# Kernel optimization log

Measured on AMD Instinct MI355X. Metric: run time of the kernel, lower is better.

## Reference

```python
import jax, jax.numpy as jnp
import numpy as np

N, L, D, H, MLP_MULT = 2, 384, 512, 8, 4
HD = D // H
DM = D * MLP_MULT
EPS = 1e-5


def _linear_params(key, out_dim, in_dim, scale=0.02):
    kw, kb = jax.random.split(key)
    w = jax.random.normal(kw, (out_dim, in_dim), jnp.float32) * scale
    b = jax.random.normal(kb, (out_dim,), jnp.float32) * scale
    return w, b


def setup_inputs() -> dict:
    key = jax.random.key(0)
    ks = jax.random.split(key, 12)
    x = jax.random.normal(ks[0], (N, L, D), jnp.float32)
    mem = jax.random.normal(ks[1], (N, L, D), jnp.float32)
    pairwise_distances = jax.random.normal(ks[2], (N, L, L, D), jnp.float32)
    mem_padding_mask = jax.random.randint(ks[3], (N, L), 0, 2).astype(bool)
    qw, qb = _linear_params(ks[4], D, D)
    kvw, kvb = _linear_params(ks[5], 2 * D, D)
    pw, pb = _linear_params(ks[6], D, D)
    edw, edb = _linear_params(ks[7], H, D)
    w1, b1 = _linear_params(ks[8], DM, D)
    w2, b2 = _linear_params(ks[9], DM, DM)
    w3, b3 = _linear_params(ks[10], D, DM)
    return {
        'x': x, 'mem': mem, 'pairwise_distances': pairwise_distances,
        'mem_padding_mask': mem_padding_mask,
        'qw': qw, 'qb': qb, 'kvw': kvw, 'kvb': kvb, 'pw': pw, 'pb': pb,
        'edw': edw, 'edb': edb,
        'ln1_g': jnp.ones((D,), jnp.float32), 'ln1_b': jnp.zeros((D,), jnp.float32),
        'ln2_g': jnp.ones((D,), jnp.float32), 'ln2_b': jnp.zeros((D,), jnp.float32),
        'w1': w1, 'b1': b1, 'w2': w2, 'b2': b2, 'w3': w3, 'b3': b3,
    }


def _layernorm(x, g, b):
    m = jnp.mean(x, axis=-1, keepdims=True)
    v = jnp.mean((x - m) ** 2, axis=-1, keepdims=True)
    return (x - m) * jax.lax.rsqrt(v + EPS) * g + b


def reference(x, mem, pairwise_distances, mem_padding_mask,
              qw, qb, kvw, kvb, pw, pb, edw, edb,
              ln1_g, ln1_b, ln2_g, ln2_b,
              w1, b1, w2, b2, w3, b3):
    scale = HD ** -0.5
    a_in = _layernorm(x, ln1_g, ln1_b)
    a_mem = _layernorm(mem, ln1_g, ln1_b)

    q = (a_in @ qw.T + qb).reshape(N, L, H, HD).transpose(0, 2, 1, 3)   # (N,H,L1,HD)
    kv = (a_mem @ kvw.T + kvb).reshape(N, L, 2, H, HD)
    k = kv[:, :, 0].transpose(0, 2, 1, 3)                               # (N,H,L2,HD)
    v = kv[:, :, 1].transpose(0, 2, 1, 3)

    scores = jnp.einsum('bhid,bhjd->bhij', q, k) * scale                # (N,H,L1,L2)

    # T5-style relative position bias from pairwise distances
    bias = (pairwise_distances @ edw.T + edb)                            # (N,L1,L2,H)
    scores = scores + bias.transpose(0, 3, 1, 2)

    # padding mask (True = padded); rows that are fully padded get a zero
    # mask instead (then their output is zeroed after attention)
    all_pad = jnp.all(mem_padding_mask, axis=-1)                         # (N,)
    neg_inf = jnp.asarray(-jnp.inf, scores.dtype)
    mask = jnp.where(mem_padding_mask[:, None, None, :], neg_inf, 0.0)
    mask = jnp.where(all_pad[:, None, None, None], 0.0, mask)
    scores = scores + mask

    attn = jax.nn.softmax(scores, axis=-1)
    out = jnp.einsum('bhij,bhjd->bhid', attn, v)                         # (N,H,L1,HD)
    out = out * (~all_pad)[:, None, None, None]
    out = out.transpose(0, 2, 1, 3).reshape(N, L, D)

    x = x + (out @ pw.T + pb)

    h = _layernorm(x, ln2_g, ln2_b)
    h = jax.nn.silu(h @ w1.T + b1)
    h = jax.nn.silu(h @ w2.T + b2)
    h = h @ w3.T + b3
    return x + h
```

## Files before the change

### kernel.cpp

```cpp
#include <hip/hip_runtime.h>
#include <hip/hip_bf16.h>
#include <math.h>

#define NB   2
#define LSEQ 384
#define DMODEL 512
#define NH   8
#define HD2  64
#define DMLP 2048
#define LL2  (LSEQ*LSEQ)
#define ROWS (NB*LSEQ)

using bf16x8 = __attribute__((ext_vector_type(8))) short;
using f32x4  = __attribute__((ext_vector_type(4))) float;

__device__ __forceinline__ unsigned short f2bf(float f) {
    union { __hip_bfloat16 h; unsigned short u; } cv;
    cv.h = __float2bfloat16(f);
    return cv.u;
}

__device__ __forceinline__ void gload_lds16(const void* g, void* l) {
    __builtin_amdgcn_global_load_lds(
        (const __attribute__((address_space(1))) void*)g,
        (__attribute__((address_space(3))) void*)l, 16, 0, 0);
}

__device__ __forceinline__ void wait_vmcnt(int rem) {
    if (rem >= 3)      asm volatile("s_waitcnt vmcnt(12)" ::: "memory");
    else if (rem == 2) asm volatile("s_waitcnt vmcnt(8)"  ::: "memory");
    else if (rem == 1) asm volatile("s_waitcnt vmcnt(4)"  ::: "memory");
    else               asm volatile("s_waitcnt vmcnt(0)"  ::: "memory");
}

__global__ __launch_bounds__(256) void cvt_all_kernel(
        const float* __restrict__ s0, const float* __restrict__ s1,
        const float* __restrict__ s2, const float* __restrict__ s3,
        const float* __restrict__ s4, const float* __restrict__ s5,
        const float* __restrict__ edw,
        unsigned short* __restrict__ d0, unsigned short* __restrict__ d1,
        unsigned short* __restrict__ d2, unsigned short* __restrict__ d3,
        unsigned short* __restrict__ d4, unsigned short* __restrict__ d5,
        unsigned short* __restrict__ edwb) {
    const int stride = gridDim.x * blockDim.x;
    const int t0 = blockIdx.x * blockDim.x + threadIdx.x;
    const float* srcs[6] = {s0, s1, s2, s3, s4, s5};
    unsigned short* dsts[6] = {d0, d1, d2, d3, d4, d5};
    const int nf4[6] = {DMODEL*DMODEL/4, 2*DMODEL*DMODEL/4, DMODEL*DMODEL/4,
                        DMLP*DMODEL/4, DMLP*DMLP/4, DMLP*DMODEL/4};
    #pragma unroll
    for (int a = 0; a < 6; a++) {
        const float* s = srcs[a];
        unsigned short* d = dsts[a];
        for (int i = t0; i < nf4[a]; i += stride) {
            float4 v = *(const float4*)(s + (size_t)i * 4);
            ushort4 o = {f2bf(v.x), f2bf(v.y), f2bf(v.z), f2bf(v.w)};
            *(ushort4*)(d + (size_t)i * 4) = o;
        }
    }
    for (int i = t0; i < 16 * 512 / 4; i += stride) {
        int row = (i * 4) >> 9;
        float4 v = {0.f, 0.f, 0.f, 0.f};
        if (row < 8) v = *(const float4*)(edw + (size_t)i * 4);
        ushort4 o = {f2bf(v.x), f2bf(v.y), f2bf(v.z), f2bf(v.w)};
        *(ushort4*)(edwb + (size_t)i * 4) = o;
    }
}

__global__ __launch_bounds__(256) void ln_kernel(const float* __restrict__ src0,
                                                 const float* __restrict__ src1,
                                                 const float* __restrict__ g,
                                                 const float* __restrict__ b,
                                                 unsigned short* __restrict__ dst0,
                                                 unsigned short* __restrict__ dst1) {
    int lane = threadIdx.x & 63;
    int row  = blockIdx.x * 4 + (threadIdx.x >> 6);
    const float* src = (row < ROWS) ? src0 : src1;
    unsigned short* dst = (row < ROWS) ? dst0 : dst1;
    int r2 = (row < ROWS) ? row : row - ROWS;
    const float* p = src + (size_t)r2 * DMODEL + lane * 8;
    float4 v0 = *(const float4*)p;
    float4 v1 = *(const float4*)(p + 4);
    float s  = v0.x + v0.y + v0.z + v0.w + v1.x + v1.y + v1.z + v1.w;
    float ss = v0.x*v0.x + v0.y*v0.y + v0.z*v0.z + v0.w*v0.w
             + v1.x*v1.x + v1.y*v1.y + v1.z*v1.z + v1.w*v1.w;
    #pragma unroll
    for (int o = 32; o; o >>= 1) { s += __shfl_xor(s, o); ss += __shfl_xor(ss, o); }
    float m   = s * (1.0f / DMODEL);
    float var = ss * (1.0f / DMODEL) - m * m;
    float r   = rsqrtf(var + 1e-5f);
    float4 g0 = *(const float4*)(g + lane * 8);
    float4 g1 = *(const float4*)(g + lane * 8 + 4);
    float4 b0 = *(const float4*)(b + lane * 8);
    float4 b1 = *(const float4*)(b + lane * 8 + 4);
    unsigned short* q = dst + (size_t)r2 * DMODEL + lane * 8;
    ushort4 lo = {f2bf((v0.x - m) * r * g0.x + b0.x), f2bf((v0.y - m) * r * g0.y + b0.y),
                  f2bf((v0.z - m) * r * g0.z + b0.z), f2bf((v0.w - m) * r * g0.w + b0.w)};
    ushort4 hi = {f2bf((v1.x - m) * r * g1.x + b1.x), f2bf((v1.y - m) * r * g1.y + b1.y),
                  f2bf((v1.z - m) * r * g1.z + b1.z), f2bf((v1.w - m) * r * g1.w + b1.w)};
    *(ushort4*)q = lo;
    *(ushort4*)(q + 4) = hi;
}

__global__ __launch_bounds__(256) void bias_mfma(const float* __restrict__ pd,
                                                 const unsigned short* __restrict__ edwb,
                                                 const float* __restrict__ edb,
                                                 const int* __restrict__ mask,
                                                 float* __restrict__ biasb) {
    __shared__ float Asb[2][64 * 64];
    const int tid = threadIdx.x;
    const int lane = tid & 63, w = tid >> 6;
    const int T = blockIdx.x;
    const size_t row0 = (size_t)T * 64;
    const int n = T / 2304;
    const int rem64 = (T - n * 2304) * 64;
    const int i = rem64 / LSEQ, j0 = rem64 % LSEQ;

    int pad = 1;
    for (int j = lane; j < LSEQ; j += 64) pad &= (mask[n * LSEQ + j] != 0) ? 1 : 0;
    unsigned long long bal = __ballot(pad);
    const int ap = (bal == ~0ull) ? 1 : 0;

    int rr[4], sc[4];
    #pragma unroll
    for (int q = 0; q < 4; q++) {
        int s = q * 256 + tid;
        rr[q] = s >> 4;
        int cs = s & 15;
        sc[q] = (cs & 8) | ((cs & 7) ^ (rr[q] & 7));
    }

    const int c = lane & 15, g = lane >> 4;
    f32x4 acc = {};

    #pragma unroll
    for (int q = 0; q < 4; q++)
        gload_lds16(pd + (row0 + rr[q]) * DMODEL + sc[q] * 4, &Asb[0][(q * 256 + tid) * 4]);
    __syncthreads();

    for (int kc = 0; kc < 8; kc++) {
        if (kc < 7) {
            const int nb = (kc + 1) & 1;
            #pragma unroll
            for (int q = 0; q < 4; q++)
                gload_lds16(pd + (row0 + rr[q]) * DMODEL + (kc + 1) * 64 + sc[q] * 4,
                            &Asb[nb][(q * 256 + tid) * 4]);
        }
        const float* Ab = &Asb[kc & 1][0];
        #pragma unroll
        for (int ks = 0; ks < 2; ks++) {
            const int ch0 = (8 * ks) | ((2 * g) ^ (c & 7));
            const int ch1 = (8 * ks) | ((2 * g + 1) ^ (c & 7));
            float4 a0 = *(const float4*)&Ab[(w * 16 + c) * 64 + ch0 * 4];
            float4 a1 = *(const float4*)&Ab[(w * 16 + c) * 64 + ch1 * 4];
            bf16x8 af;
            af[0] = (short)f2bf(a0.x); af[1] = (short)f2bf(a0.y);
            af[2] = (short)f2bf(a0.z); af[3] = (short)f2bf(a0.w);
            af[4] = (short)f2bf(a1.x); af[5] = (short)f2bf(a1.y);
            af[6] = (short)f2bf(a1.z); af[7] = (short)f2bf(a1.w);
            bf16x8 bfv = *(const bf16x8*)&edwb[c * 512 + kc * 64 + ks * 32 + g * 8];
            acc = __builtin_amdgcn_mfma_f32_16x16x32_bf16(af, bfv, acc, 0, 0, 0);
        }
        if (kc < 7) __syncthreads();
    }

    if (c < 8) {
        const float eb = edb[c];
        const int jj = j0 + w * 16 + g * 4;
        int4 mv = *(const int4*)&mask[n * LSEQ + jj];
        const float NEGINF = -__builtin_inff();
        float4 o;
        o.x = acc[0] + eb + ((!ap && mv.x) ? NEGINF : 0.0f);
        o.y = acc[1] + eb + ((!ap && mv.y) ? NEGINF : 0.0f);
        o.z = acc[2] + eb + ((!ap && mv.z) ? NEGINF : 0.0f);
        o.w = acc[3] + eb + ((!ap && mv.w) ? NEGINF : 0.0f);
        *(float4*)&biasb[(size_t)(n * 8 + c) * LL2 + (size_t)i * LSEQ + jj] = o;
    }
}

template<int ACT, int RES, int OBF>
__device__ __forceinline__ void gemm_body(const unsigned short* __restrict__ A,
        const unsigned short* __restrict__ W, const float* __restrict__ bv,
        const float* __restrict__ Rsd, void* __restrict__ Cv,
        int Nn, int K, int m0, int n0, short* As, short* Ws) {
    const int tid  = threadIdx.x;
    const int lane = tid & 63, w = tid >> 6;
    const int wr = w >> 1, wc = w & 1;
    const int s0 = tid, s1 = 256 + tid;
    const int r0 = s0 >> 3, c0 = ((s0 & 7) ^ (r0 & 7)) << 3;
    const int r1 = s1 >> 3, c1 = ((s1 & 7) ^ (r1 & 7)) << 3;
    const unsigned short* ag0 = A + (size_t)(m0 + r0) * K + c0;
    const unsigned short* ag1 = A + (size_t)(m0 + r1) * K + c1;
    const unsigned short* wg0 = W + (size_t)(n0 + r0) * K + c0;
    const unsigned short* wg1 = W + (size_t)(n0 + r1) * K + c1;

    f32x4 acc[2][2] = {};
    const int lc = lane & 15, lr = lane >> 4;
    const int KT = K >> 6;

    #pragma unroll
    for (int t = 0; t < 4; t++) {
        const int b = t * 4096, k0 = t << 6;
        gload_lds16(ag0 + k0, &As[b + s0 * 8]);
        gload_lds16(ag1 + k0, &As[b + s1 * 8]);
        gload_lds16(wg0 + k0, &Ws[b + s0 * 8]);
        gload_lds16(wg1 + k0, &Ws[b + s1 * 8]);
    }

    for (int t = 0; t < KT; t++) {
        int rem = KT - 1 - t; if (rem > 3) rem = 3;
        wait_vmcnt(rem);
        __builtin_amdgcn_s_barrier();
        __builtin_amdgcn_sched_barrier(0);
        const int cur = (t & 3) * 4096;
        bf16x8 af[2][2], bfr[2][2];
        #pragma unroll
        for (int m = 0; m < 2; m++) {
            const int rra = wr * 32 + m * 16 + lc;
            #pragma unroll
            for (int kk = 0; kk < 2; kk++) {
                const int cc = (lr + kk * 4) ^ (rra & 7);
                af[m][kk] = *(const bf16x8*)&As[cur + rra * 64 + cc * 8];
            }
        }
        #pragma unroll
        for (int nn = 0; nn < 2; nn++) {
            const int rrb = wc * 32 + nn * 16 + lc;
            #pragma unroll
            for (int kk = 0; kk < 2; kk++) {
                const int cc = (lr + kk * 4) ^ (rrb & 7);
                bfr[nn][kk] = *(const bf16x8*)&Ws[cur + rrb * 64 + cc * 8];
            }
        }
        #pragma unroll
        for (int m = 0; m < 2; m++)
            #pragma unroll
            for (int nn = 0; nn < 2; nn++) {
                acc[m][nn] = __builtin_amdgcn_mfma_f32_16x16x32_bf16(af[m][0], bfr[nn][0], acc[m][nn], 0, 0, 0);
                acc[m][nn] = __builtin_amdgcn_mfma_f32_16x16x32_bf16(af[m][1], bfr[nn][1], acc[m][nn], 0, 0, 0);
            }
        if (t + 4 < KT) {
            __builtin_amdgcn_sched_barrier(0);
            __builtin_amdgcn_s_barrier();
            const int b = cur, k0 = (t + 4) << 6;
            gload_lds16(ag0 + k0, &As[b + s0 * 8]);
            gload_lds16(ag1 + k0, &As[b + s1 * 8]);
            gload_lds16(wg0 + k0, &Ws[b + s0 * 8]);
            gload_lds16(wg1 + k0, &Ws[b + s1 * 8]);
        }
    }

    #pragma unroll
    for (int nn = 0; nn < 2; nn++) {
        int gcol = n0 + wc * 32 + nn * 16 + lc;
        float bb = bv[gcol];
        #pragma unroll
        for (int m = 0; m < 2; m++) {
            #pragma unroll
            for (int r = 0; r < 4; r++) {
                int grow = m0 + wr * 32 + m * 16 + lr * 4 + r;
                float o = acc[m][nn][r] + bb;
                if (ACT) o = o / (1.0f + expf(-o));
                if (RES) o += Rsd[(size_t)grow * Nn + gcol];
                if (OBF) ((unsigned short*)Cv)[(size_t)grow * Nn + gcol] = f2bf(o);
                else     ((float*)Cv)[(size_t)grow * Nn + gcol] = o;
            }
        }
    }
}

template<int ACT, int RES, int OBF>
__global__ __launch_bounds__(256) void mfma_gemm(const unsigned short* __restrict__ A,
                                                 const unsigned short* __restrict__ W,
                                                 const float* __restrict__ bv,
                                                 const float* __restrict__ Rsd,
                                                 void* __restrict__ Cv, int Nn, int K) {
    __shared__ short As[4 * 4096];
    __shared__ short Ws[4 * 4096];
    gemm_body<ACT, RES, OBF>(A, W, bv, Rsd, Cv, Nn, K, blockIdx.y * 64, blockIdx.x * 64, As, Ws);
}

__global__ __launch_bounds__(256) void qkv_gemm(const unsigned short* __restrict__ a_in,
                                                const unsigned short* __restrict__ a_mem,
                                                const unsigned short* __restrict__ qwb,
                                                const unsigned short* __restrict__ kvwb,
                                                const float* __restrict__ qbv,
                                                const float* __restrict__ kvbv,
                                                float* __restrict__ qbuf,
                                                float* __restrict__ kvbuf) {
    __shared__ short As[4 * 4096];
    __shared__ short Ws[4 * 4096];
    const int bx = blockIdx.x;
    const unsigned short* A; const unsigned short* W; const float* bv; float* C; int Nn, n0;
    if (bx < 8) { A = a_in;  W = qwb;  bv = qbv;  C = qbuf;  Nn = DMODEL;     n0 = bx * 64; }
    else        { A = a_mem; W = kvwb; bv = kvbv; C = kvbuf; Nn = 2 * DMODEL; n0 = (bx - 8) * 64; }
    gemm_body<0, 0, 0>(A, W, bv, nullptr, C, Nn, DMODEL, blockIdx.y * 64, n0, As, Ws);
}

__global__ __launch_bounds__(256) void scores_kernel(const float* __restrict__ q,
                                                     const float* __restrict__ kv,
                                                     const float* __restrict__ biasb,
                                                     float* __restrict__ S) {
    const int n = blockIdx.z, h = blockIdx.y;
    const int it = blockIdx.x / 12, jt = blockIdx.x % 12;
    __shared__ float Qs[64][32];
    __shared__ float Ks[64][32];
    const int tid = threadIdx.x;
    const int r = tid >> 3, c = (tid & 7) << 3;
    {
        const float* qp = q + ((size_t)(n * LSEQ + it * 32 + r)) * DMODEL + h * HD2 + c;
        float4 q0 = *(const float4*)qp;
        float4 q1 = *(const float4*)(qp + 4);
        Qs[c+0][r]=q0.x; Qs[c+1][r]=q0.y; Qs[c+2][r]=q0.z; Qs[c+3][r]=q0.w;
        Qs[c+4][r]=q1.x; Qs[c+5][r]=q1.y; Qs[c+6][r]=q1.z; Qs[c+7][r]=q1.w;
        const float* kp = kv + ((size_t)(n * LSEQ + jt * 32 + r)) * (2 * DMODEL) + h * HD2 + c;
        float4 k0 = *(const float4*)kp;
        float4 k1 = *(const float4*)(kp + 4);
        Ks[c+0][r]=k0.x; Ks[c+1][r]=k0.y; Ks[c+2][r]=k0.z; Ks[c+3][r]=k0.w;
        Ks[c+4][r]=k1.x; Ks[c+5][r]=k1.y; Ks[c+6][r]=k1.z; Ks[c+7][r]=k1.w;
    }
    __syncthreads();
    const int tx = tid & 15, ty = tid >> 4;
    float acc[2][2] = {{0.f,0.f},{0.f,0.f}};
    #pragma unroll
    for (int k = 0; k < 64; k++) {
        float2 a  = *(const float2*)&Qs[k][ty << 1];
        float2 b2 = *(const float2*)&Ks[k][tx << 1];
        acc[0][0] = fmaf(a.x, b2.x, acc[0][0]);
        acc[0][1] = fmaf(a.x, b2.y, acc[0][1]);
        acc[1][0] = fmaf(a.y, b2.x, acc[1][0]);
        acc[1][1] = fmaf(a.y, b2.y, acc[1][1]);
    }
    #pragma unroll
    for (int i2 = 0; i2 < 2; i2++) {
        int gi = it * 32 + (ty << 1) + i2;
        #pragma unroll
        for (int j2 = 0; j2 < 2; j2++) {
            int gj = jt * 32 + (tx << 1) + j2;
            size_t idx = ((size_t)(n * 8 + h)) * LL2 + (size_t)gi * LSEQ + gj;
            S[idx] = acc[i2][j2] * 0.125f + biasb[idx];
        }
    }
}

__global__ __launch_bounds__(256) void softmax_kernel(float* __restrict__ S) {
    int lane = threadIdx.x & 63;
    int row  = blockIdx.x * 4 + (threadIdx.x >> 6);
    float* p = S + (size_t)row * LSEQ;
    float v[6];
    #pragma unroll
    for (int cc = 0; cc < 6; cc++) v[cc] = p[cc * 64 + lane];
    float mx = v[0];
    #pragma unroll
    for (int cc = 1; cc < 6; cc++) mx = fmaxf(mx, v[cc]);
    #pragma unroll
    for (int o = 32; o; o >>= 1) mx = fmaxf(mx, __shfl_xor(mx, o));
    float sum = 0.f;
    #pragma unroll
    for (int cc = 0; cc < 6; cc++) { v[cc] = expf(v[cc] - mx); sum += v[cc]; }
    #pragma unroll
    for (int o = 32; o; o >>= 1) sum += __shfl_xor(sum, o);
    float inv = 1.0f / sum;
    #pragma unroll
    for (int cc = 0; cc < 6; cc++) p[cc * 64 + lane] = v[cc] * inv;
}

__global__ __launch_bounds__(256) void av_kernel(const float* __restrict__ S,
                                                 const float* __restrict__ kv,
                                                 const int* __restrict__ mask,
                                                 unsigned short* __restrict__ outb) {
    const int it = blockIdx.x, h = blockIdx.y, n = blockIdx.z;
    __shared__ float Ps[32][68];
    __shared__ float Vs[64][68];
    const int tid = threadIdx.x;
    const int lane = tid & 63;
    int pad = 1;
    for (int j = lane; j < LSEQ; j += 64) pad &= (mask[n * LSEQ + j] != 0) ? 1 : 0;
    unsigned long long bal = __ballot(pad != 0);
    const float zf = (bal == 0xFFFFFFFFFFFFFFFFull) ? 0.0f : 1.0f;
    const int tx = tid & 15, ty = tid >> 4;
    const int pr = tid >> 3, pc = (tid & 7) << 3;
    const int vr = tid >> 2, vc = (tid & 3) << 4;
    float acc0[4] = {0,0,0,0}, acc1[4] = {0,0,0,0};
    for (int j0 = 0; j0 < LSEQ; j0 += 64) {
        const float* sp = S + ((size_t)(n * 8 + h)) * LL2 + (size_t)(it * 32 + pr) * LSEQ + j0 + pc;
        float4 p0 = *(const float4*)sp;
        float4 p1 = *(const float4*)(sp + 4);
        *(float4*)&Ps[pr][pc]     = p0;
        *(float4*)&Ps[pr][pc + 4] = p1;
        #pragma unroll
        for (int u = 0; u < 4; u++) {
            float4 vvv = *(const float4*)&kv[((size_t)(n * LSEQ + j0 + vr)) * (2 * DMODEL)
                                             + DMODEL + h * HD2 + vc + 4 * u];
            *(float4*)&Vs[vr][vc + 4 * u] = vvv;
        }
        __syncthreads();
        #pragma unroll
        for (int j = 0; j < 64; j++) {
            float pa  = Ps[ty][j];
            float pb2 = Ps[ty + 16][j];
            float4 vv = *(const float4*)&Vs[j][tx << 2];
            acc0[0] = fmaf(pa,  vv.x, acc0[0]);
            acc0[1] = fmaf(pa,  vv.y, acc0[1]);
            acc0[2] = fmaf(pa,  vv.z, acc0[2]);
            acc0[3] = fmaf(pa,  vv.w, acc0[3]);
            acc1[0] = fmaf(pb2, vv.x, acc1[0]);
            acc1[1] = fmaf(pb2, vv.y, acc1[1]);
            acc1[2] = fmaf(pb2, vv.z, acc1[2]);
            acc1[3] = fmaf(pb2, vv.w, acc1[3]);
        }
        __syncthreads();
    }
    int i0 = it * 32;
    ushort4 o0 = {f2bf(acc0[0]*zf), f2bf(acc0[1]*zf), f2bf(acc0[2]*zf), f2bf(acc0[3]*zf)};
    ushort4 o1 = {f2bf(acc1[0]*zf), f2bf(acc1[1]*zf), f2bf(acc1[2]*zf), f2bf(acc1[3]*zf)};
    *(ushort4*)&outb[((size_t)(n * LSEQ + i0 + ty)) * DMODEL + h * HD2 + (tx << 2)]      = o0;
    *(ushort4*)&outb[((size_t)(n * LSEQ + i0 + ty + 16)) * DMODEL + h * HD2 + (tx << 2)] = o1;
}

extern "C" void kernel_launch(void* const* d_in, const int* in_sizes, int n_in,
                              void* d_out, int out_size, void* d_ws, size_t ws_size,
                              hipStream_t stream) {
    const float* x    = (const float*)d_in[0];
    const float* mem  = (const float*)d_in[1];
    const float* pd   = (const float*)d_in[2];
    const int*   mask = (const int*)d_in[3];
    const float* qw   = (const float*)d_in[4];
    const float* qbv  = (const float*)d_in[5];
    const float* kvw  = (const float*)d_in[6];
    const float* kvbv = (const float*)d_in[7];
    const float* pw   = (const float*)d_in[8];
    const float* pbv  = (const float*)d_in[9];
    const float* edw  = (const float*)d_in[10];
    const float* edb  = (const float*)d_in[11];
    const float* ln1g = (const float*)d_in[12];
    const float* ln1b = (const float*)d_in[13];
    const float* ln2g = (const float*)d_in[14];
    const float* ln2b = (const float*)d_in[15];
    const float* w1   = (const float*)d_in[16];
    const float* b1   = (const float*)d_in[17];
    const float* w2   = (const float*)d_in[18];
    const float* b2   = (const float*)d_in[19];
    const float* w3   = (const float*)d_in[20];
    const float* b3   = (const float*)d_in[21];

    float* wsf = (float*)d_ws;
    float* biasb  = wsf + 16;
    float* scores = biasb + (size_t)NB * NH * LL2;
    float* qbuf   = scores + (size_t)NB * NH * LL2;
    float* kvbuf  = qbuf + (size_t)ROWS * DMODEL;
    float* x1buf  = kvbuf + (size_t)ROWS * 2 * DMODEL;
    unsigned short* a_in  = (unsigned short*)(x1buf + (size_t)ROWS * DMODEL);
    unsigned short* a_mem = a_in  + (size_t)ROWS * DMODEL;
    unsigned short* attno = a_mem + (size_t)ROWS * DMODEL;
    unsigned short* h0    = attno + (size_t)ROWS * DMODEL;
    unsigned short* h1    = h0    + (size_t)ROWS * DMODEL;
    unsigned short* h2    = h1    + (size_t)ROWS * DMLP;
    unsigned short* qwb   = h2    + (size_t)ROWS * DMLP;
    unsigned short* kvwb  = qwb   + (size_t)DMODEL * DMODEL;
    unsigned short* pwb   = kvwb  + (size_t)2 * DMODEL * DMODEL;
    unsigned short* w1b   = pwb   + (size_t)DMODEL * DMODEL;
    unsigned short* w2b   = w1b   + (size_t)DMLP * DMODEL;
    unsigned short* w3b   = w2b   + (size_t)DMLP * DMLP;
    unsigned short* edwb  = w3b   + (size_t)DMLP * DMODEL;

    float* outp = (float*)d_out;

    cvt_all_kernel<<<2048, 256, 0, stream>>>(qw, kvw, pw, w1, w2, w3, edw,
                                             qwb, kvwb, pwb, w1b, w2b, w3b, edwb);
    ln_kernel<<<2 * ROWS / 4, 256, 0, stream>>>(x, mem, ln1g, ln1b, a_in, a_mem);
    bias_mfma<<<NB * LL2 / 64, 256, 0, stream>>>(pd, edwb, edb, mask, biasb);

    qkv_gemm<<<dim3(24, 12), 256, 0, stream>>>(a_in, a_mem, qwb, kvwb, qbv, kvbv, qbuf, kvbuf);

    scores_kernel<<<dim3(144, NH, NB), 256, 0, stream>>>(qbuf, kvbuf, biasb, scores);
    softmax_kernel<<<(NB * NH * LSEQ) / 4, 256, 0, stream>>>(scores);
    av_kernel<<<dim3(12, NH, NB), 256, 0, stream>>>(scores, kvbuf, mask, attno);

    mfma_gemm<0,1,0><<<dim3(DMODEL/64, ROWS/64), 256, 0, stream>>>(attno, pwb, pbv, x, x1buf, DMODEL, DMODEL);
    ln_kernel<<<ROWS / 4, 256, 0, stream>>>(x1buf, x1buf, ln2g, ln2b, h0, h0);
    mfma_gemm<1,0,1><<<dim3(DMLP/64, ROWS/64), 256, 0, stream>>>(h0, w1b, b1, nullptr, h1, DMLP, DMODEL);
    mfma_gemm<1,0,1><<<dim3(DMLP/64, ROWS/64), 256, 0, stream>>>(h1, w2b, b2, nullptr, h2, DMLP, DMLP);
    mfma_gemm<0,1,0><<<dim3(DMODEL/64, ROWS/64), 256, 0, stream>>>(h2, w3b, b3, x1buf, outp, DMODEL, DMLP);
}
```

Before: 264.2 us.

## Fuse attention into flash-style kernel, merge prep kernels, widen MLP GEMM tiles

Replaces the separate scores, softmax and AV kernels with one online-softmax attention kernel, so the full fp32 score matrix no longer has to be written and reread. Merges the first layernorm into the weight-conversion kernel to save a launch. Triple-buffers the bias projection and keeps its edw fragments in registers. Adds a 64x128-tile, triple-buffered GEMM for the two wide MLP layers. The fused attention runs only 192 blocks with scalar FMA math, which may leave the GPU underused, and the extra registers and LDS could lower occupancy.

After: 295.5 us. +11.8%, slower.

```diff
diff --git a/kernel.cpp b/kernel.cpp
--- a/kernel.cpp
+++ b/kernel.cpp
@@ -26,14 +26,10 @@
         (__attribute__((address_space(3))) void*)l, 16, 0, 0);
 }
 
-__device__ __forceinline__ void wait_vmcnt(int rem) {
-    if (rem >= 3)      asm volatile("s_waitcnt vmcnt(12)" ::: "memory");
-    else if (rem == 2) asm volatile("s_waitcnt vmcnt(8)"  ::: "memory");
-    else if (rem == 1) asm volatile("s_waitcnt vmcnt(4)"  ::: "memory");
-    else               asm volatile("s_waitcnt vmcnt(0)"  ::: "memory");
-}
-
-__global__ __launch_bounds__(256) void cvt_all_kernel(
+__global__ __launch_bounds__(256) void pre_kernel(
+        const float* __restrict__ x, const float* __restrict__ mem,
+        const float* __restrict__ ln1g, const float* __restrict__ ln1b,
+        unsigned short* __restrict__ a_in, unsigned short* __restrict__ a_mem,
         const float* __restrict__ s0, const float* __restrict__ s1,
         const float* __restrict__ s2, const float* __restrict__ s3,
         const float* __restrict__ s4, const float* __restrict__ s5,
@@ -42,8 +38,39 @@
         unsigned short* __restrict__ d2, unsigned short* __restrict__ d3,
         unsigned short* __restrict__ d4, unsigned short* __restrict__ d5,
         unsigned short* __restrict__ edwb) {
-    const int stride = gridDim.x * blockDim.x;
-    const int t0 = blockIdx.x * blockDim.x + threadIdx.x;
+    const int tid = threadIdx.x;
+    if (blockIdx.x < 384) {
+        int lane = tid & 63;
+        int row  = blockIdx.x * 4 + (tid >> 6);
+        const float* src = (row < ROWS) ? x : mem;
+        unsigned short* dst = (row < ROWS) ? a_in : a_mem;
+        int r2 = (row < ROWS) ? row : row - ROWS;
+        const float* p = src + (size_t)r2 * DMODEL + lane * 8;
+        float4 v0 = *(const float4*)p;
+        float4 v1 = *(const float4*)(p + 4);
+        float s  = v0.x + v0.y + v0.z + v0.w + v1.x + v1.y + v1.z + v1.w;
+        float ss = v0.x*v0.x + v0.y*v0.y + v0.z*v0.z + v0.w*v0.w
+                 + v1.x*v1.x + v1.y*v1.y + v1.z*v1.z + v1.w*v1.w;
+        #pragma unroll
+        for (int o = 32; o; o >>= 1) { s += __shfl_xor(s, o); ss += __shfl_xor(ss, o); }
+        float m   = s * (1.0f / DMODEL);
+        float var = ss * (1.0f / DMODEL) - m * m;
+        float r   = rsqrtf(var + 1e-5f);
+        float4 g0 = *(const float4*)(ln1g + lane * 8);
+        float4 g1 = *(const float4*)(ln1g + lane * 8 + 4);
+        float4 b0 = *(const float4*)(ln1b + lane * 8);
+        float4 b1 = *(const float4*)(ln1b + lane * 8 + 4);
+        unsigned short* q = dst + (size_t)r2 * DMODEL + lane * 8;
+        ushort4 lo = {f2bf((v0.x-m)*r*g0.x+b0.x), f2bf((v0.y-m)*r*g0.y+b0.y),
+                      f2bf((v0.z-m)*r*g0.z+b0.z), f2bf((v0.w-m)*r*g0.w+b0.w)};
+        ushort4 hi = {f2bf((v1.x-m)*r*g1.x+b1.x), f2bf((v1.y-m)*r*g1.y+b1.y),
+                      f2bf((v1.z-m)*r*g1.z+b1.z), f2bf((v1.w-m)*r*g1.w+b1.w)};
+        *(ushort4*)q = lo;
+        *(ushort4*)(q + 4) = hi;
+        return;
+    }
+    const int stride = (gridDim.x - 384) * 256;
+    const int t0 = (blockIdx.x - 384) * 256 + tid;
     const float* srcs[6] = {s0, s1, s2, s3, s4, s5};
     unsigned short* dsts[6] = {d0, d1, d2, d3, d4, d5};
     const int nf4[6] = {DMODEL*DMODEL/4, 2*DMODEL*DMODEL/4, DMODEL*DMODEL/4,
@@ -59,7 +86,7 @@
         }
     }
     for (int i = t0; i < 16 * 512 / 4; i += stride) {
-        int row = (i * 4) >> 9;
+        int row = i >> 7;
         float4 v = {0.f, 0.f, 0.f, 0.f};
         if (row < 8) v = *(const float4*)(edw + (size_t)i * 4);
         ushort4 o = {f2bf(v.x), f2bf(v.y), f2bf(v.z), f2bf(v.w)};
@@ -68,17 +95,12 @@
 }
 
 __global__ __launch_bounds__(256) void ln_kernel(const float* __restrict__ src0,
-                                                 const float* __restrict__ src1,
                                                  const float* __restrict__ g,
                                                  const float* __restrict__ b,
-                                                 unsigned short* __restrict__ dst0,
-                                                 unsigned short* __restrict__ dst1) {
+                                                 unsigned short* __restrict__ dst0) {
     int lane = threadIdx.x & 63;
     int row  = blockIdx.x * 4 + (threadIdx.x >> 6);
-    const float* src = (row < ROWS) ? src0 : src1;
-    unsigned short* dst = (row < ROWS) ? dst0 : dst1;
-    int r2 = (row < ROWS) ? row : row - ROWS;
-    const float* p = src + (size_t)r2 * DMODEL + lane * 8;
+    const float* p = src0 + (size_t)row * DMODEL + lane * 8;
     float4 v0 = *(const float4*)p;
     float4 v1 = *(const float4*)(p + 4);
     float s  = v0.x + v0.y + v0.z + v0.w + v1.x + v1.y + v1.z + v1.w;
@@ -93,11 +115,11 @@
     float4 g1 = *(const float4*)(g + lane * 8 + 4);
     float4 b0 = *(const float4*)(b + lane * 8);
     float4 b1 = *(const float4*)(b + lane * 8 + 4);
-    unsigned short* q = dst + (size_t)r2 * DMODEL + lane * 8;
-    ushort4 lo = {f2bf((v0.x - m) * r * g0.x + b0.x), f2bf((v0.y - m) * r * g0.y + b0.y),
-                  f2bf((v0.z - m) * r * g0.z + b0.z), f2bf((v0.w - m) * r * g0.w + b0.w)};
-    ushort4 hi = {f2bf((v1.x - m) * r * g1.x + b1.x), f2bf((v1.y - m) * r * g1.y + b1.y),
-                  f2bf((v1.z - m) * r * g1.z + b1.z), f2bf((v1.w - m) * r * g1.w + b1.w)};
+    unsigned short* q = dst0 + (size_t)row * DMODEL + lane * 8;
+    ushort4 lo = {f2bf((v0.x-m)*r*g0.x+b0.x), f2bf((v0.y-m)*r*g0.y+b0.y),
+                  f2bf((v0.z-m)*r*g0.z+b0.z), f2bf((v0.w-m)*r*g0.w+b0.w)};
+    ushort4 hi = {f2bf((v1.x-m)*r*g1.x+b1.x), f2bf((v1.y-m)*r*g1.y+b1.y),
+                  f2bf((v1.z-m)*r*g1.z+b1.z), f2bf((v1.w-m)*r*g1.w+b1.w)};
     *(ushort4*)q = lo;
     *(ushort4*)(q + 4) = hi;
 }
@@ -107,7 +129,7 @@
                                                  const float* __restrict__ edb,
                                                  const int* __restrict__ mask,
                                                  float* __restrict__ biasb) {
-    __shared__ float Asb[2][64 * 64];
+    __shared__ float Asb[3][64 * 64];
     const int tid = threadIdx.x;
     const int lane = tid & 63, w = tid >> 6;
     const int T = blockIdx.x;
@@ -116,6 +138,14 @@
     const int rem64 = (T - n * 2304) * 64;
     const int i = rem64 / LSEQ, j0 = rem64 % LSEQ;
 
+    const int c = lane & 15, g = lane >> 4;
+    bf16x8 bfv[8][2];
+    #pragma unroll
+    for (int kc = 0; kc < 8; kc++)
+        #pragma unroll
+        for (int ks = 0; ks < 2; ks++)
+            bfv[kc][ks] = *(const bf16x8*)&edwb[c * 512 + kc * 64 + ks * 32 + g * 8];
+
     int pad = 1;
     for (int j = lane; j < LSEQ; j += 64) pad &= (mask[n * LSEQ + j] != 0) ? 1 : 0;
     unsigned long long bal = __ballot(pad);
@@ -130,23 +160,29 @@
         sc[q] = (cs & 8) | ((cs & 7) ^ (rr[q] & 7));
     }
 
-    const int c = lane & 15, g = lane >> 4;
     f32x4 acc = {};
 
     #pragma unroll
     for (int q = 0; q < 4; q++)
         gload_lds16(pd + (row0 + rr[q]) * DMODEL + sc[q] * 4, &Asb[0][(q * 256 + tid) * 4]);
-    __syncthreads();
-
+    #pragma unroll
+    for (int q = 0; q < 4; q++)
+        gload_lds16(pd + (row0 + rr[q]) * DMODEL + 64 + sc[q] * 4, &Asb[1][(q * 256 + tid) * 4]);
+
+    #pragma unroll
     for (int kc = 0; kc < 8; kc++) {
-        if (kc < 7) {
-            const int nb = (kc + 1) & 1;
+        if (kc < 7) asm volatile("s_waitcnt vmcnt(16)" ::: "memory");
+        else        asm volatile("s_waitcnt vmcnt(0)"  ::: "memory");
+        __builtin_amdgcn_s_barrier();
+        __builtin_amdgcn_sched_barrier(0);
+        if (kc + 2 < 8) {
+            const int nb = (kc + 2) % 3;
             #pragma unroll
             for (int q = 0; q < 4; q++)
-                gload_lds16(pd + (row0 + rr[q]) * DMODEL + (kc + 1) * 64 + sc[q] * 4,
+                gload_lds16(pd + (row0 + rr[q]) * DMODEL + (kc + 2) * 64 + sc[q] * 4,
                             &Asb[nb][(q * 256 + tid) * 4]);
         }
-        const float* Ab = &Asb[kc & 1][0];
+        const float* Ab = &Asb[kc % 3][0];
         #pragma unroll
         for (int ks = 0; ks < 2; ks++) {
             const int ch0 = (8 * ks) | ((2 * g) ^ (c & 7));
@@ -158,10 +194,8 @@
             af[2] = (short)f2bf(a0.z); af[3] = (short)f2bf(a0.w);
             af[4] = (short)f2bf(a1.x); af[5] = (short)f2bf(a1.y);
             af[6] = (short)f2bf(a1.z); af[7] = (short)f2bf(a1.w);
-            bf16x8 bfv = *(const bf16x8*)&edwb[c * 512 + kc * 64 + ks * 32 + g * 8];
-            acc = __builtin_amdgcn_mfma_f32_16x16x32_bf16(af, bfv, acc, 0, 0, 0);
-        }
-        if (kc < 7) __syncthreads();
+            acc = __builtin_amdgcn_mfma_f32_16x16x32_bf16(af, bfv[kc][ks], acc, 0, 0, 0);
+        }
     }
 
     if (c < 8) {
@@ -209,7 +243,10 @@
 
     for (int t = 0; t < KT; t++) {
         int rem = KT - 1 - t; if (rem > 3) rem = 3;
-        wait_vmcnt(rem);
+        if (rem >= 3)      asm volatile("s_waitcnt vmcnt(12)" ::: "memory");
+        else if (rem == 2) asm volatile("s_waitcnt vmcnt(8)"  ::: "memory");
+        else if (rem == 1) asm volatile("s_waitcnt vmcnt(4)"  ::: "memory");
+        else               asm volatile("s_waitcnt vmcnt(0)"  ::: "memory");
         __builtin_amdgcn_s_barrier();
         __builtin_amdgcn_sched_barrier(0);
         const int cur = (t & 3) * 4096;
@@ -297,106 +334,193 @@
     gemm_body<0, 0, 0>(A, W, bv, nullptr, C, Nn, DMODEL, blockIdx.y * 64, n0, As, Ws);
 }
 
-__global__ __launch_bounds__(256) void scores_kernel(const float* __restrict__ q,
-                                                     const float* __restrict__ kv,
-                                                     const float* __restrict__ biasb,
-                                                     float* __restrict__ S) {
-    const int n = blockIdx.z, h = blockIdx.y;
-    const int it = blockIdx.x / 12, jt = blockIdx.x % 12;
-    __shared__ float Qs[64][32];
-    __shared__ float Ks[64][32];
-    const int tid = threadIdx.x;
-    const int r = tid >> 3, c = (tid & 7) << 3;
-    {
-        const float* qp = q + ((size_t)(n * LSEQ + it * 32 + r)) * DMODEL + h * HD2 + c;
-        float4 q0 = *(const float4*)qp;
-        float4 q1 = *(const float4*)(qp + 4);
-        Qs[c+0][r]=q0.x; Qs[c+1][r]=q0.y; Qs[c+2][r]=q0.z; Qs[c+3][r]=q0.w;
-        Qs[c+4][r]=q1.x; Qs[c+5][r]=q1.y; Qs[c+6][r]=q1.z; Qs[c+7][r]=q1.w;
-        const float* kp = kv + ((size_t)(n * LSEQ + jt * 32 + r)) * (2 * DMODEL) + h * HD2 + c;
-        float4 k0 = *(const float4*)kp;
-        float4 k1 = *(const float4*)(kp + 4);
-        Ks[c+0][r]=k0.x; Ks[c+1][r]=k0.y; Ks[c+2][r]=k0.z; Ks[c+3][r]=k0.w;
-        Ks[c+4][r]=k1.x; Ks[c+5][r]=k1.y; Ks[c+6][r]=k1.z; Ks[c+7][r]=k1.w;
-    }
-    __syncthreads();
-    const int tx = tid & 15, ty = tid >> 4;
-    float acc[2][2] = {{0.f,0.f},{0.f,0.f}};
-    #pragma unroll
-    for (int k = 0; k < 64; k++) {
-        float2 a  = *(const float2*)&Qs[k][ty << 1];
-        float2 b2 = *(const float2*)&Ks[k][tx << 1];
-        acc[0][0] = fmaf(a.x, b2.x, acc[0][0]);
-        acc[0][1] = fmaf(a.x, b2.y, acc[0][1]);
-        acc[1][0] = fmaf(a.y, b2.x, acc[1][0]);
-        acc[1][1] = fmaf(a.y, b2.y, acc[1][1]);
-    }
-    #pragma unroll
-    for (int i2 = 0; i2 < 2; i2++) {
-        int gi = it * 32 + (ty << 1) + i2;
-        #pragma unroll
-        for (int j2 = 0; j2 < 2; j2++) {
-            int gj = jt * 32 + (tx << 1) + j2;
-            size_t idx = ((size_t)(n * 8 + h)) * LL2 + (size_t)gi * LSEQ + gj;
-            S[idx] = acc[i2][j2] * 0.125f + biasb[idx];
-        }
-    }
-}
-
-__global__ __launch_bounds__(256) void softmax_kernel(float* __restrict__ S) {
-    int lane = threadIdx.x & 63;
-    int row  = blockIdx.x * 4 + (threadIdx.x >> 6);
-    float* p = S + (size_t)row * LSEQ;
-    float v[6];
-    #pragma unroll
-    for (int cc = 0; cc < 6; cc++) v[cc] = p[cc * 64 + lane];
-    float mx = v[0];
-    #pragma unroll
-    for (int cc = 1; cc < 6; cc++) mx = fmaxf(mx, v[cc]);
-    #pragma unroll
-    for (int o = 32; o; o >>= 1) mx = fmaxf(mx, __shfl_xor(mx, o));
-    float sum = 0.f;
-    #pragma unroll
-    for (int cc = 0; cc < 6; cc++) { v[cc] = expf(v[cc] - mx); sum += v[cc]; }
-    #pragma unroll
-    for (int o = 32; o; o >>= 1) sum += __shfl_xor(sum, o);
-    float inv = 1.0f / sum;
-    #pragma unroll
-    for (int cc = 0; cc < 6; cc++) p[cc * 64 + lane] = v[cc] * inv;
-}
-
-__global__ __launch_bounds__(256) void av_kernel(const float* __restrict__ S,
-                                                 const float* __restrict__ kv,
-                                                 const int* __restrict__ mask,
-                                                 unsigned short* __restrict__ outb) {
+template<int ACT, int RES, int OBF>
+__global__ __launch_bounds__(256) void mfma_gemm128(const unsigned short* __restrict__ A,
+                                                    const unsigned short* __restrict__ W,
+                                                    const float* __restrict__ bv,
+                                                    const float* __restrict__ Rsd,
+                                                    void* __restrict__ Cv, int Nn, int K) {
+    __shared__ short As[3 * 4096];
+    __shared__ short Ws[3 * 8192];
+    const int tid = threadIdx.x, lane = tid & 63, w = tid >> 6;
+    const int wm = w >> 1, wn = w & 1;
+    const int m0 = blockIdx.y * 64, n0 = blockIdx.x * 128;
+    const int ar0 = tid >> 3, ac0 = ((tid & 7) ^ (ar0 & 7)) << 3;
+    const int ar1 = (256 + tid) >> 3, ac1 = (((256 + tid) & 7) ^ (ar1 & 7)) << 3;
+    int brr[4], bcc[4];
+    #pragma unroll
+    for (int q = 0; q < 4; q++) {
+        int s = q * 256 + tid;
+        brr[q] = s >> 3;
+        bcc[q] = ((s & 7) ^ (brr[q] & 7)) << 3;
+    }
+    const unsigned short* ag0 = A + (size_t)(m0 + ar0) * K + ac0;
+    const unsigned short* ag1 = A + (size_t)(m0 + ar1) * K + ac1;
+
+    f32x4 acc[2][4] = {};
+    const int lc = lane & 15, lr = lane >> 4;
+    const int KT = K >> 6;
+
+    #pragma unroll
+    for (int t = 0; t < 2; t++) {
+        const int ab = t * 4096, bb = t * 8192, k0 = t << 6;
+        gload_lds16(ag0 + k0, &As[ab + tid * 8]);
+        gload_lds16(ag1 + k0, &As[ab + (256 + tid) * 8]);
+        #pragma unroll
+        for (int q = 0; q < 4; q++)
+            gload_lds16(W + (size_t)(n0 + brr[q]) * K + k0 + bcc[q],
+                        &Ws[bb + (q * 256 + tid) * 8]);
+    }
+
+    for (int t = 0; t < KT; t++) {
+        if (t < KT - 1) asm volatile("s_waitcnt vmcnt(6)" ::: "memory");
+        else            asm volatile("s_waitcnt vmcnt(0)" ::: "memory");
+        __builtin_amdgcn_s_barrier();
+        __builtin_amdgcn_sched_barrier(0);
+        if (t + 2 < KT) {
+            const int nb = (t + 2) % 3, k0 = (t + 2) << 6;
+            gload_lds16(ag0 + k0, &As[nb * 4096 + tid * 8]);
+            gload_lds16(ag1 + k0, &As[nb * 4096 + (256 + tid) * 8]);
+            #pragma unroll
+            for (int q = 0; q < 4; q++)
+                gload_lds16(W + (size_t)(n0 + brr[q]) * K + k0 + bcc[q],
+                            &Ws[nb * 8192 + (q * 256 + tid) * 8]);
+        }
+        const int ca = (t % 3) * 4096, cb = (t % 3) * 8192;
+        bf16x8 af[2][2], bfr[4][2];
+        #pragma unroll
+        for (int m = 0; m < 2; m++) {
+            const int rra = wm * 32 + m * 16 + lc;
+            #pragma unroll
+            for (int kk = 0; kk < 2; kk++) {
+                const int cc = (lr + kk * 4) ^ (rra & 7);
+                af[m][kk] = *(const bf16x8*)&As[ca + rra * 64 + cc * 8];
+            }
+        }
+        #pragma unroll
+        for (int nn = 0; nn < 4; nn++) {
+            const int rrb = wn * 64 + nn * 16 + lc;
+            #pragma unroll
+            for (int kk = 0; kk < 2; kk++) {
+                const int cc = (lr + kk * 4) ^ (rrb & 7);
+                bfr[nn][kk] = *(const bf16x8*)&Ws[cb + rrb * 64 + cc * 8];
+            }
+        }
+        #pragma unroll
+        for (int m = 0; m < 2; m++)
+            #pragma unroll
+            for (int nn = 0; nn < 4; nn++) {
+                acc[m][nn] = __builtin_amdgcn_mfma_f32_16x16x32_bf16(af[m][0], bfr[nn][0], acc[m][nn], 0, 0, 0);
+                acc[m][nn] = __builtin_amdgcn_mfma_f32_16x16x32_bf16(af[m][1], bfr[nn][1], acc[m][nn], 0, 0, 0);
+            }
+        __builtin_amdgcn_sched_barrier(0);
+        __builtin_amdgcn_s_barrier();
+    }
+
+    #pragma unroll
+    for (int nn = 0; nn < 4; nn++) {
+        int gcol = n0 + wn * 64 + nn * 16 + lc;
+        float bb = bv[gcol];
+        #pragma unroll
+        for (int m = 0; m < 2; m++) {
+            #pragma unroll
+            for (int r = 0; r < 4; r++) {
+                int grow = m0 + wm * 32 + m * 16 + lr * 4 + r;
+                float o = acc[m][nn][r] + bb;
+                if (ACT) o = o / (1.0f + expf(-o));
+                if (RES) o += Rsd[(size_t)grow * Nn + gcol];
+                if (OBF) ((unsigned short*)Cv)[(size_t)grow * Nn + gcol] = f2bf(o);
+                else     ((float*)Cv)[(size_t)grow * Nn + gcol] = o;
+            }
+        }
+    }
+}
+
+__global__ __launch_bounds__(256) void attn_kernel(const float* __restrict__ qb,
+                                                   const float* __restrict__ kvb,
+                                                   const float* __restrict__ biasb,
+                                                   const int* __restrict__ mask,
+                                                   unsigned short* __restrict__ outb) {
+    __shared__ float Qs[64][33];
+    __shared__ float Ks[64][33];
+    __shared__ float Vs[32][66];
+    __shared__ float Ps[32][33];
+    __shared__ float rowscale[32];
+    __shared__ float rowl[32];
     const int it = blockIdx.x, h = blockIdx.y, n = blockIdx.z;
-    __shared__ float Ps[32][68];
-    __shared__ float Vs[64][68];
     const int tid = threadIdx.x;
     const int lane = tid & 63;
     int pad = 1;
     for (int j = lane; j < LSEQ; j += 64) pad &= (mask[n * LSEQ + j] != 0) ? 1 : 0;
     unsigned long long bal = __ballot(pad != 0);
-    const float zf = (bal == 0xFFFFFFFFFFFFFFFFull) ? 0.0f : 1.0f;
+    const float zf = (bal == ~0ull) ? 0.0f : 1.0f;
+
+    const int r = tid >> 3, c = (tid & 7) << 3;
+    {
+        const float* qp = qb + ((size_t)(n * LSEQ + it * 32 + r)) * DMODEL + h * HD2 + c;
+        float4 q0 = *(const float4*)qp;
+        float4 q1 = *(const float4*)(qp + 4);
+        Qs[c+0][r]=q0.x; Qs[c+1][r]=q0.y; Qs[c+2][r]=q0.z; Qs[c+3][r]=q0.w;
+        Qs[c+4][r]=q1.x; Qs[c+5][r]=q1.y; Qs[c+6][r]=q1.z; Qs[c+7][r]=q1.w;
+    }
     const int tx = tid & 15, ty = tid >> 4;
-    const int pr = tid >> 3, pc = (tid & 7) << 3;
-    const int vr = tid >> 2, vc = (tid & 3) << 4;
+    float mr0 = -3.0e38f, mr1 = -3.0e38f, l0 = 0.f, l1 = 0.f;
     float acc0[4] = {0,0,0,0}, acc1[4] = {0,0,0,0};
-    for (int j0 = 0; j0 < LSEQ; j0 += 64) {
-        const float* sp = S + ((size_t)(n * 8 + h)) * LL2 + (size_t)(it * 32 + pr) * LSEQ + j0 + pc;
-        float4 p0 = *(const float4*)sp;
-        float4 p1 = *(const float4*)(sp + 4);
-        *(float4*)&Ps[pr][pc]     = p0;
-        *(float4*)&Ps[pr][pc + 4] = p1;
-        #pragma unroll
-        for (int u = 0; u < 4; u++) {
-            float4 vvv = *(const float4*)&kv[((size_t)(n * LSEQ + j0 + vr)) * (2 * DMODEL)
-                                             + DMODEL + h * HD2 + vc + 4 * u];
-            *(float4*)&Vs[vr][vc + 4 * u] = vvv;
-        }
+    const size_t sbase = ((size_t)(n * 8 + h)) * LL2;
+
+    for (int jt = 0; jt < 12; jt++) {
         __syncthreads();
-        #pragma unroll
-        for (int j = 0; j < 64; j++) {
+        {
+            const float* kp = kvb + ((size_t)(n * LSEQ + jt * 32 + r)) * (2 * DMODEL) + h * HD2 + c;
+            float4 k0 = *(const float4*)kp;
+            float4 k1 = *(const float4*)(kp + 4);
+            Ks[c+0][r]=k0.x; Ks[c+1][r]=k0.y; Ks[c+2][r]=k0.z; Ks[c+3][r]=k0.w;
+            Ks[c+4][r]=k1.x; Ks[c+5][r]=k1.y; Ks[c+6][r]=k1.z; Ks[c+7][r]=k1.w;
+            const float* vp = kp + DMODEL;
+            float4 v0 = *(const float4*)vp;
+            float4 v1 = *(const float4*)(vp + 4);
+            *(float4*)&Vs[r][c]     = v0;
+            *(float4*)&Vs[r][c + 4] = v1;
+        }
+        __syncthreads();
+        float s00 = 0.f, s01 = 0.f, s10 = 0.f, s11 = 0.f;
+        #pragma unroll
+        for (int k = 0; k < 64; k++) {
+            float2 a  = *(const float2*)&Qs[k][ty << 1];
+            float2 b2 = *(const float2*)&Ks[k][tx << 1];
+            s00 = fmaf(a.x, b2.x, s00); s01 = fmaf(a.x, b2.y, s01);
+            s10 = fmaf(a.y, b2.x, s10); s11 = fmaf(a.y, b2.y, s11);
+        }
+        const int gi0 = it * 32 + (ty << 1);
+        const int gj  = jt * 32 + (tx << 1);
+        const float* bp = &biasb[sbase + (size_t)gi0 * LSEQ + gj];
+        float2 b0 = *(const float2*)bp;
+        float2 b1 = *(const float2*)(bp + LSEQ);
+        s00 = fmaf(s00, 0.125f, b0.x); s01 = fmaf(s01, 0.125f, b0.y);
+        s10 = fmaf(s10, 0.125f, b1.x); s11 = fmaf(s11, 0.125f, b1.y);
+        float t0 = fmaxf(s00, s01), t1 = fmaxf(s10, s11);
+        #pragma unroll
+        for (int o = 8; o; o >>= 1) { t0 = fmaxf(t0, __shfl_xor(t0, o)); t1 = fmaxf(t1, __shfl_xor(t1, o)); }
+        float mn0 = fmaxf(mr0, t0), mn1 = fmaxf(mr1, t1);
+        float sc0 = __expf(mr0 - mn0), sc1 = __expf(mr1 - mn1);
+        float p00 = __expf(s00 - mn0), p01 = __expf(s01 - mn0);
+        float p10 = __expf(s10 - mn1), p11 = __expf(s11 - mn1);
+        float ts0 = p00 + p01, ts1 = p10 + p11;
+        #pragma unroll
+        for (int o = 8; o; o >>= 1) { ts0 += __shfl_xor(ts0, o); ts1 += __shfl_xor(ts1, o); }
+        l0 = l0 * sc0 + ts0; l1 = l1 * sc1 + ts1;
+        mr0 = mn0; mr1 = mn1;
+        if (tx == 0) { rowscale[(ty << 1)] = sc0; rowscale[(ty << 1) + 1] = sc1; }
+        Ps[(ty << 1)][(tx << 1)]     = p00;
+        Ps[(ty << 1)][(tx << 1) + 1] = p01;
+        Ps[(ty << 1) + 1][(tx << 1)]     = p10;
+        Ps[(ty << 1) + 1][(tx << 1) + 1] = p11;
+        __syncthreads();
+        float rs0 = rowscale[ty], rs1 = rowscale[ty + 16];
+        #pragma unroll
+        for (int u = 0; u < 4; u++) { acc0[u] *= rs0; acc1[u] *= rs1; }
+        #pragma unroll
+        for (int j = 0; j < 32; j++) {
             float pa  = Ps[ty][j];
             float pb2 = Ps[ty + 16][j];
             float4 vv = *(const float4*)&Vs[j][tx << 2];
@@ -409,11 +533,13 @@
             acc1[2] = fmaf(pb2, vv.z, acc1[2]);
             acc1[3] = fmaf(pb2, vv.w, acc1[3]);
         }
-        __syncthreads();
-    }
-    int i0 = it * 32;
-    ushort4 o0 = {f2bf(acc0[0]*zf), f2bf(acc0[1]*zf), f2bf(acc0[2]*zf), f2bf(acc0[3]*zf)};
-    ushort4 o1 = {f2bf(acc1[0]*zf), f2bf(acc1[1]*zf), f2bf(acc1[2]*zf), f2bf(acc1[3]*zf)};
+    }
+    if (tx == 0) { rowl[(ty << 1)] = l0; rowl[(ty << 1) + 1] = l1; }
+    __syncthreads();
+    float inv0 = zf / rowl[ty], inv1 = zf / rowl[ty + 16];
+    const int i0 = it * 32;
+    ushort4 o0 = {f2bf(acc0[0]*inv0), f2bf(acc0[1]*inv0), f2bf(acc0[2]*inv0), f2bf(acc0[3]*inv0)};
+    ushort4 o1 = {f2bf(acc1[0]*inv1), f2bf(acc1[1]*inv1), f2bf(acc1[2]*inv1), f2bf(acc1[3]*inv1)};
     *(ushort4*)&outb[((size_t)(n * LSEQ + i0 + ty)) * DMODEL + h * HD2 + (tx << 2)]      = o0;
     *(ushort4*)&outb[((size_t)(n * LSEQ + i0 + ty + 16)) * DMODEL + h * HD2 + (tx << 2)] = o1;
 }
@@ -446,8 +572,7 @@
 
     float* wsf = (float*)d_ws;
     float* biasb  = wsf + 16;
-    float* scores = biasb + (size_t)NB * NH * LL2;
-    float* qbuf   = scores + (size_t)NB * NH * LL2;
+    float* qbuf   = biasb + (size_t)NB * NH * LL2;
     float* kvbuf  = qbuf + (size_t)ROWS * DMODEL;
     float* x1buf  = kvbuf + (size_t)ROWS * 2 * DMODEL;
     unsigned short* a_in  = (unsigned short*)(x1buf + (size_t)ROWS * DMODEL);
@@ -466,20 +591,15 @@
 
     float* outp = (float*)d_out;
 
-    cvt_all_kernel<<<2048, 256, 0, stream>>>(qw, kvw, pw, w1, w2, w3, edw,
-                                             qwb, kvwb, pwb, w1b, w2b, w3b, edwb);
-    ln_kernel<<<2 * ROWS / 4, 256, 0, stream>>>(x, mem, ln1g, ln1b, a_in, a_mem);
+    pre_kernel<<<2048, 256, 0, stream>>>(x, mem, ln1g, ln1b, a_in, a_mem,
+                                         qw, kvw, pw, w1, w2, w3, edw,
+                                         qwb, kvwb, pwb, w1b, w2b, w3b, edwb);
     bias_mfma<<<NB * LL2 / 64, 256, 0, stream>>>(pd, edwb, edb, mask, biasb);
-
     qkv_gemm<<<dim3(24, 12), 256, 0, stream>>>(a_in, a_mem, qwb, kvwb, qbv, kvbv, qbuf, kvbuf);
-
-    scores_kernel<<<dim3(144, NH, NB), 256, 0, stream>>>(qbuf, kvbuf, biasb, scores);
-    softmax_kernel<<<(NB * NH * LSEQ) / 4, 256, 0, stream>>>(scores);
-    av_kernel<<<dim3(12, NH, NB), 256, 0, stream>>>(scores, kvbuf, mask, attno);
-
-    mfma_gemm<0,1,0><<<dim3(DMODEL/64, ROWS/64), 256, 0, stream>>>(attno, pwb, pbv, x, x1buf, DMODEL, DMODEL);
-    ln_kernel<<<ROWS / 4, 256, 0, stream>>>(x1buf, x1buf, ln2g, ln2b, h0, h0);
-    mfma_gemm<1,0,1><<<dim3(DMLP/64, ROWS/64), 256, 0, stream>>>(h0, w1b, b1, nullptr, h1, DMLP, DMODEL);
-    mfma_gemm<1,0,1><<<dim3(DMLP/64, ROWS/64), 256, 0, stream>>>(h1, w2b, b2, nullptr, h2, DMLP, DMLP);
-    mfma_gemm<0,1,0><<<dim3(DMODEL/64, ROWS/64), 256, 0, stream>>>(h2, w3b, b3, x1buf, outp, DMODEL, DMLP);
-}
+    attn_kernel<<<dim3(12, NH, NB), 256, 0, stream>>>(qbuf, kvbuf, biasb, mask, attno);
+    mfma_gemm<0,1,0><<<dim3(8, 12), 256, 0, stream>>>(attno, pwb, pbv, x, x1buf, DMODEL, DMODEL);
+    ln_kernel<<<ROWS / 4, 256, 0, stream>>>(x1buf, ln2g, ln2b, h0);
+    mfma_gemm128<1,0,1><<<dim3(16, 12), 256, 0, stream>>>(h0, w1b, b1, nullptr, h1, DMLP, DMODEL);
+    mfma_gemm128<1,0,1><<<dim3(16, 12), 256, 0, stream>>>(h1, w2b, b2, nullptr, h2, DMLP, DMLP);
+    mfma_gemm<0,1,0><<<dim3(8, 12), 256, 0, stream>>>(h2, w3b, b3, x1buf, outp, DMODEL, DMLP);
+}
```
